# Performance work log

Hardware: AMD Instinct MI355X
Metric: run time of the kernel (lower is better)

## Reference

```python
import jax, jax.numpy as jnp
import numpy as np

B, S, D, H, L, F = 2, 2048, 512, 8, 6, 2048
MAX = 5000
HD = D // H
OFF = MAX - 1


def _layernorm(x, g, b, eps=1e-5):
    m = jnp.mean(x, axis=-1, keepdims=True)
    v = jnp.mean((x - m) ** 2, axis=-1, keepdims=True)
    return (x - m) / jnp.sqrt(v + eps) * g + b


def _sinusoidal_pe(seq_len, d_model):
    pos = jnp.arange(seq_len, dtype=jnp.float32)[:, None]
    div = jnp.exp(jnp.arange(0, d_model, 2, dtype=jnp.float32) * (-np.log(10000.0) / d_model))
    pe = jnp.zeros((seq_len, d_model), jnp.float32)
    pe = pe.at[:, 0::2].set(jnp.sin(pos * div))
    pe = pe.at[:, 1::2].set(jnp.cos(pos * div))
    return pe


def setup_inputs() -> dict:
    key = jax.random.key(0)
    ks = iter(jax.random.split(key, 64))

    def n(shape, s):
        return (jax.random.normal(next(ks), shape, jnp.float32) * s).astype(jnp.float32)

    inp = {}
    inp['x'] = jax.random.normal(next(ks), (B, S, D), jnp.float32)
    inp['f0'] = jax.random.normal(next(ks), (B, S, 1), jnp.float32)
    inp['sp'] = jax.random.normal(next(ks), (B, S, 1), jnp.float32)
    inp['ap'] = jax.random.normal(next(ks), (B, S, 1), jnp.float32)
    inp['spk_emb'] = jax.random.normal(next(ks), (B, D), jnp.float32)
    # conditional positional encoding projections (weights stored as (in,out); y = x @ W + b)
    inp['Wf0'] = n((1, D), 0.1); inp['bf0'] = jnp.zeros((D,), jnp.float32)
    inp['Wsp'] = n((1, D), 0.1); inp['bsp'] = jnp.zeros((D,), jnp.float32)
    inp['Wap'] = n((1, D), 0.1); inp['bap'] = jnp.zeros((D,), jnp.float32)
    inp['Wspk'] = n((D, D), 0.02); inp['bspk'] = jnp.zeros((D,), jnp.float32)
    # per-layer stacked params
    inp['Wq'] = n((L, D, D), 0.02); inp['bq'] = jnp.zeros((L, D), jnp.float32)
    inp['Wk'] = n((L, D, D), 0.02); inp['bk'] = jnp.zeros((L, D), jnp.float32)
    inp['Wv'] = n((L, D, D), 0.02); inp['bv'] = jnp.zeros((L, D), jnp.float32)
    inp['Wo'] = n((L, D, D), 0.02); inp['bo'] = jnp.zeros((L, D), jnp.float32)
    inp['ln1_g'] = jnp.ones((L, D), jnp.float32); inp['ln1_b'] = jnp.zeros((L, D), jnp.float32)
    inp['ln2_g'] = jnp.ones((L, D), jnp.float32); inp['ln2_b'] = jnp.zeros((L, D), jnp.float32)
    inp['W1'] = n((L, D, F), 0.02); inp['b1'] = jnp.zeros((L, F), jnp.float32)
    inp['W2'] = n((L, F, D), 0.02); inp['b2'] = jnp.zeros((L, D), jnp.float32)
    inp['rel_table'] = n((L, 2 * MAX - 1, H), 0.02)
    inp['gfin'] = jnp.ones((D,), jnp.float32); inp['bfin'] = jnp.zeros((D,), jnp.float32)
    return inp


def _forward(x, f0, sp, ap, spk_emb,
             Wf0, bf0, Wsp, bsp, Wap, bap, Wspk, bspk,
             Wq, bq, Wk, bk, Wv, bv, Wo, bo,
             ln1_g, ln1_b, ln2_g, ln2_b, W1, b1, W2, b2,
             rel_table, gfin, bfin):
    # --- conditional positional encoding (dropout = identity, eval mode) ---
    x = x + _sinusoidal_pe(S, D)[None]
    x = x + (f0 @ Wf0 + bf0)
    x = x + (sp @ Wsp + bsp)
    x = x + (ap @ Wap + bap)
    spk = jnp.broadcast_to(spk_emb[:, None, :], (B, S, D))
    x = x + (spk @ Wspk + bspk)

    # relative coords: added bias for (query q, key k) is table[k - q + OFF] (matches transpose(1,3) in torch)
    coords = jnp.arange(S)
    rel = jnp.clip(coords[None, :] - coords[:, None] + OFF, 0, 2 * MAX - 2)  # (S_q, S_k)

    scale = 1.0 / np.sqrt(HD)

    def layer(x, p):
        (Wq_, bq_, Wk_, bk_, Wv_, bv_, Wo_, bo_,
         g1, be1, g2, be2, W1_, b1_, W2_, b2_, tab) = p
        res = x
        h = _layernorm(x, g1, be1)
        Q = (h @ Wq_ + bq_).reshape(B, S, H, HD)
        K = (h @ Wk_ + bk_).reshape(B, S, H, HD)
        V = (h @ Wv_ + bv_).reshape(B, S, H, HD)
        scores = jnp.einsum('bqhd,bkhd->bhqk', Q, K) * scale
        bias = jnp.transpose(tab[rel], (2, 0, 1))  # (H, S_q, S_k)
        scores = scores + bias[None]
        attn = jax.nn.softmax(scores, axis=-1)
        ao = jnp.einsum('bhqk,bkhd->bqhd', attn, V).reshape(B, S, D)
        x = res + (ao @ Wo_ + bo_)
        res = x
        h = _layernorm(x, g2, be2)
        h = jax.nn.gelu(h @ W1_ + b1_, approximate=False)
        x = res + (h @ W2_ + b2_)
        return x, None

    params = (Wq, bq, Wk, bk, Wv, bv, Wo, bo,
              ln1_g, ln1_b, ln2_g, ln2_b, W1, b1, W2, b2, rel_table)
    x, _ = jax.lax.scan(layer, x, params)
    return _layernorm(x, gfin, bfin)


def reference(x, f0, sp, ap, spk_emb,
              Wf0, bf0, Wsp, bsp, Wap, bap, Wspk, bspk,
              Wq, bq, Wk, bk, Wv, bv, Wo, bo,
              ln1_g, ln1_b, ln2_g, ln2_b, W1, b1, W2, b2,
              rel_table, gfin, bfin):
    return _forward(x, f0, sp, ap, spk_emb,
                    Wf0, bf0, Wsp, bsp, Wap, bap, Wspk, bspk,
                    Wq, bq, Wk, bk, Wv, bv, Wo, bo,
                    ln1_g, ln1_b, ln2_g, ln2_b, W1, b1, W2, b2,
                    rel_table, gfin, bfin)
```

## Files before the change

### kernel.cpp

```cpp
#include <hip/hip_runtime.h>
#include <hip/hip_bf16.h>

#define B_ 2
#define S_ 2048
#define D_ 512
#define H_ 8
#define L_ 6
#define F_ 2048
#define HD_ 64
#define M_ 4096
#define OFF_ 4999
#define NREL_ 9999

typedef short s8v __attribute__((ext_vector_type(8)));
typedef float f4v __attribute__((ext_vector_type(4)));

enum { MODE_BF16 = 0, MODE_RES = 1, MODE_GELU = 2 };

__device__ __forceinline__ short f2bf(float f) {
  unsigned u = __float_as_uint(f);
  unsigned r = (u + 0x7fffu + ((u >> 16) & 1u)) >> 16;
  return (short)r;
}

__device__ __forceinline__ float exp2fast(float x) {
  float r;
  asm("v_exp_f32 %0, %1" : "=v"(r) : "v"(x));
  return r;
}

__device__ __forceinline__ int cvt_pk_bf16(float lo, float hi) {
  int r;
  asm("v_cvt_pk_bf16_f32 %0, %1, %2" : "=v"(r) : "v"(lo), "v"(hi));
  return r;
}

__device__ __forceinline__ void gload16(const void* g, const void* l) {
  __builtin_amdgcn_global_load_lds((const __attribute__((address_space(1))) unsigned int*)g,
                                   (__attribute__((address_space(3))) unsigned int*)l,
                                   16, 0, 0);
}

__global__ void transpose_kernel(const float* __restrict__ src, short* __restrict__ dst,
                                 int K, int N, long srcBS, long dstBS, int rowOff)
{
  __shared__ float t[32][33];
  int tx = threadIdx.x, ty = threadIdx.y;
  int n0 = blockIdx.x * 32, k0 = blockIdx.y * 32, l = blockIdx.z;
  const float* s = src + (size_t)l * srcBS;
  short* d = dst + (size_t)l * dstBS;
  for (int j = 0; j < 4; ++j)
    t[ty + j*8][tx] = s[(size_t)(k0 + ty + j*8) * N + n0 + tx];
  __syncthreads();
  for (int j = 0; j < 4; ++j)
    d[(size_t)(rowOff + n0 + ty + j*8) * K + k0 + tx] = f2bf(t[tx][ty + j*8]);
}

__global__ void packb_kernel(const float* __restrict__ bq, const float* __restrict__ bk,
                             const float* __restrict__ bv, float* __restrict__ bqkv)
{
  int i = blockIdx.x * 256 + threadIdx.x;
  if (i >= L_ * 1536) return;
  int l = i / 1536, j = i % 1536;
  float v = (j < 512) ? bq[l*512 + j] : (j < 1024) ? bk[l*512 + j - 512] : bv[l*512 + j - 1024];
  bqkv[i] = v;
}

__global__ void tabt_kernel(const float* __restrict__ tab, float* __restrict__ tabT)
{
  int i = blockIdx.x * 256 + threadIdx.x;
  if (i >= L_ * H_ * NREL_) return;
  int l = i / (H_ * NREL_), rem = i % (H_ * NREL_);
  int h = rem / NREL_, idx = rem % NREL_;
  tabT[i] = tab[((size_t)l * NREL_ + idx) * H_ + h] * 1.44269504f;
}

__global__ __launch_bounds__(256) void spk_kernel(const float* __restrict__ spk,
                                                  const float* __restrict__ Wspk,
                                                  const float* __restrict__ bspk,
                                                  float* __restrict__ sproj)
{
  __shared__ float red[4][64];
  int b = blockIdx.x, nb = blockIdx.y;
  int dl = threadIdx.x & 63, kc = threadIdx.x >> 6;
  int d = nb * 64 + dl;
  const float* sprow = spk + b * D_;
  float a0 = 0.f, a1 = 0.f;
  int kbeg = kc * 128;
  for (int k = kbeg; k < kbeg + 128; k += 2) {
    a0 += sprow[k]     * Wspk[(size_t)k * D_ + d];
    a1 += sprow[k + 1] * Wspk[(size_t)(k + 1) * D_ + d];
  }
  red[kc][dl] = a0 + a1;
  __syncthreads();
  if (kc == 0)
    sproj[b*D_ + d] = red[0][dl] + red[1][dl] + red[2][dl] + red[3][dl] + bspk[d];
}

__global__ __launch_bounds__(256) void prologue_kernel(
    const float* __restrict__ x, const float* __restrict__ f0, const float* __restrict__ sp,
    const float* __restrict__ ap, const float* __restrict__ Wf0, const float* __restrict__ bf0,
    const float* __restrict__ Wsp, const float* __restrict__ bsp,
    const float* __restrict__ Wap, const float* __restrict__ bap,
    const float* __restrict__ sproj, float* __restrict__ X)
{
  int row = blockIdx.x, tid = threadIdx.x;
  int b = row >> 11, s = row & 2047;
  float vf0 = f0[row], vsp = sp[row], vap = ap[row];
  for (int j = 0; j < 2; ++j) {
    int d = tid + j * 256;
    int i = d >> 1;
    float div = expf((float)(2*i) * -0.01798894603f);
    float arg = (float)s * div;
    float pe = (d & 1) ? cosf(arg) : sinf(arg);
    float v = x[(size_t)row*D_ + d] + pe
            + vf0*Wf0[d] + bf0[d] + vsp*Wsp[d] + bsp[d] + vap*Wap[d] + bap[d]
            + sproj[b*D_ + d];
    X[(size_t)row*D_ + d] = v;
  }
}

__global__ __launch_bounds__(256) void ln_kernel(
    const float* __restrict__ X, const float* __restrict__ g, const float* __restrict__ bta,
    short* __restrict__ outB, float* __restrict__ outF, int f32out)
{
  __shared__ float red[8];
  int row = blockIdx.x, tid = threadIdx.x;
  const float* xr = X + (size_t)row * D_;
  float v0 = xr[tid], v1 = xr[tid + 256];
  float s = v0 + v1, q = v0*v0 + v1*v1;
  for (int off = 1; off < 64; off <<= 1) { s += __shfl_xor(s, off); q += __shfl_xor(q, off); }
  int w = tid >> 6;
  if ((tid & 63) == 0) { red[w*2] = s; red[w*2 + 1] = q; }
  __syncthreads();
  s = red[0] + red[2] + red[4] + red[6];
  q = red[1] + red[3] + red[5] + red[7];
  float mean = s * (1.0f / D_);
  float var = q * (1.0f / D_) - mean * mean;
  float rstd = rsqrtf(var + 1e-5f);
  float o0 = (v0 - mean) * rstd * g[tid] + bta[tid];
  float o1 = (v1 - mean) * rstd * g[tid + 256] + bta[tid + 256];
  if (f32out) {
    outF[(size_t)row*D_ + tid] = o0; outF[(size_t)row*D_ + tid + 256] = o1;
  } else {
    outB[(size_t)row*D_ + tid] = f2bf(o0); outB[(size_t)row*D_ + tid + 256] = f2bf(o1);
  }
}

template<int MODE>
__device__ __forceinline__ void gemm_body(
    const short* __restrict__ A, const short* __restrict__ Wt,
    const float* __restrict__ bias, int K, int N,
    float* outF, short* outB)
{
  __shared__ short sA[2][4096];
  __shared__ short sB[2][2048];
  const int tid = threadIdx.x;
  const int w = tid >> 6, lane = tid & 63;
  const int col = lane & 15, quad = lane >> 4;
  const int m0 = blockIdx.x * 128, n0 = blockIdx.y * 64;
  const int nkt = K >> 6;

  const int rowT = tid >> 2, kcA = tid & 3;
  const size_t kc8 = kcA * 8;

  f4v acc[2][4] = {};
  for (int kt = 0; kt < nkt; ++kt) {
    const int k0 = kt * 64;
    __syncthreads();
    for (int p = 0; p < 2; ++p) {
      gload16(A + (size_t)(m0 + rowT) * K + k0 + p*32 + kc8,       &sA[p][(w*16) * 32]);
      gload16(A + (size_t)(m0 + 64 + rowT) * K + k0 + p*32 + kc8,  &sA[p][(64 + w*16) * 32]);
      gload16(Wt + (size_t)(n0 + rowT) * K + k0 + p*32 + kc8,      &sB[p][(w*16) * 32]);
    }
    __syncthreads();
    for (int p = 0; p < 2; ++p) {
      s8v af[2], bfr[4];
      for (int mt = 0; mt < 2; ++mt)
        af[mt] = *(const s8v*)&sA[p][(w*32 + mt*16 + col) * 32 + quad * 8];
      for (int nt = 0; nt < 4; ++nt)
        bfr[nt] = *(const s8v*)&sB[p][(nt*16 + col) * 32 + quad * 8];
      for (int mt = 0; mt < 2; ++mt)
        for (int nt = 0; nt < 4; ++nt)
          acc[mt][nt] = __builtin_amdgcn_mfma_f32_16x16x32_bf16(af[mt], bfr[nt], acc[mt][nt], 0, 0, 0);
    }
  }

  const float qsc = (MODE == MODE_BF16 && n0 < 512) ? 0.18033688f : 1.0f;
  float bz[4];
  for (int nt = 0; nt < 4; ++nt)
    bz[nt] = bias[n0 + nt*16 + col];
  for (int mt = 0; mt < 2; ++mt) {
    int mbase = m0 + w*32 + mt*16 + quad*4;
    for (int nt = 0; nt < 4; ++nt) {
      int n = n0 + nt*16 + col;
      for (int r = 0; r < 4; ++r) {
        float v = acc[mt][nt][r] + bz[nt];
        size_t idx = (size_t)(mbase + r) * N + n;
        if (MODE == MODE_RES) {
          outF[idx] = outF[idx] + v;
        } else if (MODE == MODE_GELU) {
          outB[idx] = f2bf(0.5f * v * (1.0f + erff(v * 0.70710678118f)));
        } else {
          outB[idx] = f2bf(v * qsc);
        }
      }
    }
  }
}

__global__ __launch_bounds__(256) void gemm_qkv_kernel(
    const short* __restrict__ A, const short* __restrict__ Wt,
    const float* __restrict__ bias, float* outF, short* outB)
{ gemm_body<MODE_BF16>(A, Wt, bias, 512, 1536, outF, outB); }

__global__ __launch_bounds__(256) void gemm_o_kernel(
    const short* __restrict__ A, const short* __restrict__ Wt,
    const float* __restrict__ bias, float* outF, short* outB)
{ gemm_body<MODE_RES>(A, Wt, bias, 512, 512, outF, outB); }

__global__ __launch_bounds__(256) void gemm_ffn1_kernel(
    const short* __restrict__ A, const short* __restrict__ Wt,
    const float* __restrict__ bias, float* outF, short* outB)
{ gemm_body<MODE_GELU>(A, Wt, bias, 512, 2048, outF, outB); }

__global__ __launch_bounds__(256) void gemm_ffn2_kernel(
    const short* __restrict__ A, const short* __restrict__ Wt,
    const float* __restrict__ bias, float* outF, short* outB)
{ gemm_body<MODE_RES>(A, Wt, bias, 2048, 512, outF, outB); }

__global__ __launch_bounds__(256) void vtrans_kernel(const short* __restrict__ QKV,
                                                     short* __restrict__ Vt)
{
  __shared__ short t[64 * 72];
  int tid = threadIdx.x;
  int s0 = blockIdx.x * 64, bh = blockIdx.y;
  int b = bh >> 3, h = bh & 7;
  for (int it = 0; it < 2; ++it) {
    int c = it * 256 + tid;
    int sR = c >> 3, hc = c & 7;
    s8v v = *(const s8v*)(QKV + (size_t)(b*S_ + s0 + sR) * 1536 + 1024 + h*64 + hc*8);
    *(s8v*)&t[sR * 72 + hc * 8] = v;
  }
  __syncthreads();
  for (int it = 0; it < 2; ++it) {
    int c = it * 256 + tid;
    int hd = c >> 3, sc = c & 7;
    s8v v;
    for (int j = 0; j < 8; ++j) v[j] = t[(sc*8 + j) * 72 + hd];
    *(s8v*)(Vt + (size_t)(bh*64 + hd) * S_ + s0 + sc*8) = v;
  }
}

#define SM_MT(ko, mt, ST, Bb0, Bb1, Bb2, Bb3) do {                  \
    float p0 = exp2fast(ST[0] + Bb0);                               \
    float p1 = exp2fast(ST[1] + Bb1);                               \
    float p2 = exp2fast(ST[2] + Bb2);                               \
    float p3 = exp2fast(ST[3] + Bb3);                               \
    lsum += (p0 + p1) + (p2 + p3);                                  \
    int2 pk;                                                        \
    pk.x = cvt_pk_bf16(p0, p1);                                     \
    pk.y = cvt_pk_bf16(p2, p3);                                     \
    *(int2*)&sP[w*1280 + (ko)*640 + col*40 + (mt)*16 + quad*4] = pk;\
  } while (0)

#define KOBLOCK(ko, B0a,B0b,B0c,B0d, B1a,B1b,B1c,B1d) do {                         \
    f4v st0 = {}, st1 = {};                                                        \
    s8v a00 = *(const s8v*)&sK[(ko)*2560 + 0*1280 + (0*16 + col)*40 + quad*8];     \
    s8v a01 = *(const s8v*)&sK[(ko)*2560 + 1*1280 + (0*16 + col)*40 + quad*8];     \
    s8v a10 = *(const s8v*)&sK[(ko)*2560 + 0*1280 + (1*16 + col)*40 + quad*8];     \
    s8v a11 = *(const s8v*)&sK[(ko)*2560 + 1*1280 + (1*16 + col)*40 + quad*8];     \
    st0 = __builtin_amdgcn_mfma_f32_16x16x32_bf16(a00, bQ0, st0, 0, 0, 0);         \
    st0 = __builtin_amdgcn_mfma_f32_16x16x32_bf16(a01, bQ1, st0, 0, 0, 0);         \
    st1 = __builtin_amdgcn_mfma_f32_16x16x32_bf16(a10, bQ0, st1, 0, 0, 0);         \
    st1 = __builtin_amdgcn_mfma_f32_16x16x32_bf16(a11, bQ1, st1, 0, 0, 0);         \
    SM_MT(ko, 0, st0, B0a,B0b,B0c,B0d);                                            \
    SM_MT(ko, 1, st1, B1a,B1b,B1c,B1d);                                            \
    s8v aP = *(const s8v*)&sP[w*1280 + (ko)*640 + col*40 + quad*8];                \
    s8v v0 = *(const s8v*)&sV[(ko)*2560 + ( 0 + col)*40 + quad*8];                 \
    s8v v1 = *(const s8v*)&sV[(ko)*2560 + (16 + col)*40 + quad*8];                 \
    s8v v2 = *(const s8v*)&sV[(ko)*2560 + (32 + col)*40 + quad*8];                 \
    s8v v3 = *(const s8v*)&sV[(ko)*2560 + (48 + col)*40 + quad*8];                 \
    o0 = __builtin_amdgcn_mfma_f32_16x16x32_bf16(aP, v0, o0, 0, 0, 0);             \
    o1 = __builtin_amdgcn_mfma_f32_16x16x32_bf16(aP, v1, o1, 0, 0, 0);             \
    o2 = __builtin_amdgcn_mfma_f32_16x16x32_bf16(aP, v2, o2, 0, 0, 0);             \
    o3 = __builtin_amdgcn_mfma_f32_16x16x32_bf16(aP, v3, o3, 0, 0, 0);             \
  } while (0)

__global__ __launch_bounds__(512) void flash_kernel(
    const short* __restrict__ QKV, const short* __restrict__ Vt,
    const float* __restrict__ tabT, short* __restrict__ AO)
{
  __shared__ __attribute__((aligned(16))) short sK[2 * 2 * 32 * 40];
  __shared__ __attribute__((aligned(16))) short sV[2 * 64 * 40];
  __shared__ __attribute__((aligned(16))) short sP[8 * 2 * 16 * 40];
  __shared__ float sRow[8 * 16];

  const int tid = threadIdx.x;
  const int w = tid >> 6, lane = tid & 63;
  const int col = lane & 15, quad = lane >> 4;
  const int bh = blockIdx.x, qt = blockIdx.y;
  const int b = bh >> 3, h = bh & 7;
  const int q0 = qt * 128;
  const int wq = w * 16;
  const int nkt = S_ / 64;
  const float* tabh = tabT + (size_t)h * NREL_;
  const float* tbL = tabh + (OFF_ - q0 + quad*4 - wq - col);

  const short* gQ = QKV + (size_t)(b*S_ + q0 + wq + col) * 1536 + h*64 + quad*8;
  s8v bQ0 = *(const s8v*)gQ;
  s8v bQ1 = *(const s8v*)(gQ + 32);

  const int c4 = tid & 3;
  const int kK = (tid >> 2) & 63, hcK = tid >> 8;
  const short* gK = QKV + (size_t)(b*S_ + kK) * 1536 + 512 + h*64 + hcK*32 + c4*8;
  short* dK = &sK[(kK >> 5)*2560 + hcK*1280 + (kK & 31)*40 + c4*8];
  const int c8 = tid & 7, hdV = tid >> 3;
  const short* gV = Vt + (size_t)(bh*64 + hdV) * S_ + c8*8;
  short* dV = &sV[(c8 >> 2)*2560 + hdV*40 + (c8 & 3)*8];

  int4 rk = *(const int4*)gK;
  int4 rv = *(const int4*)gV;

  float lsum = 0.0f;
  f4v o0 = {}, o1 = {}, o2 = {}, o3 = {};

  for (int kt = 0; kt < nkt; ++kt) {
    const float* tb = tbL + kt * 64;
    float bA0 = tb[0],  bA1 = tb[1],  bA2 = tb[2],  bA3 = tb[3];
    float bB0 = tb[16], bB1 = tb[17], bB2 = tb[18], bB3 = tb[19];
    float bC0 = tb[32], bC1 = tb[33], bC2 = tb[34], bC3 = tb[35];
    float bD0 = tb[48], bD1 = tb[49], bD2 = tb[50], bD3 = tb[51];
    __syncthreads();
    *(int4*)dK = rk;
    *(int4*)dV = rv;
    __syncthreads();
    if (kt + 1 < nkt) {
      rk = *(const int4*)(gK + (size_t)(kt + 1) * 64 * 1536);
      rv = *(const int4*)(gV + (kt + 1) * 64);
    }
    KOBLOCK(0, bA0, bA1, bA2, bA3, bB0, bB1, bB2, bB3);
    KOBLOCK(1, bC0, bC1, bC2, bC3, bD0, bD1, bD2, bD3);
  }

  lsum += __shfl_xor(lsum, 16);
  lsum += __shfl_xor(lsum, 32);
  if (lane < 16) sRow[w*16 + lane] = lsum;
  float rs0 = sRow[w*16 + quad*4 + 0];
  float rs1 = sRow[w*16 + quad*4 + 1];
  float rs2 = sRow[w*16 + quad*4 + 2];
  float rs3 = sRow[w*16 + quad*4 + 3];
  size_t mrow = (size_t)(b*S_ + q0 + wq + quad*4);
  short* aoBase = AO + mrow * 512 + h*64 + col;
  aoBase[0*512 +  0] = f2bf(o0[0] / rs0);
  aoBase[1*512 +  0] = f2bf(o0[1] / rs1);
  aoBase[2*512 +  0] = f2bf(o0[2] / rs2);
  aoBase[3*512 +  0] = f2bf(o0[3] / rs3);
  aoBase[0*512 + 16] = f2bf(o1[0] / rs0);
  aoBase[1*512 + 16] = f2bf(o1[1] / rs1);
  aoBase[2*512 + 16] = f2bf(o1[2] / rs2);
  aoBase[3*512 + 16] = f2bf(o1[3] / rs3);
  aoBase[0*512 + 32] = f2bf(o2[0] / rs0);
  aoBase[1*512 + 32] = f2bf(o2[1] / rs1);
  aoBase[2*512 + 32] = f2bf(o2[2] / rs2);
  aoBase[3*512 + 32] = f2bf(o2[3] / rs3);
  aoBase[0*512 + 48] = f2bf(o3[0] / rs0);
  aoBase[1*512 + 48] = f2bf(o3[1] / rs1);
  aoBase[2*512 + 48] = f2bf(o3[2] / rs2);
  aoBase[3*512 + 48] = f2bf(o3[3] / rs3);
}

extern "C" void kernel_launch(void* const* d_in, const int* in_sizes, int n_in,
                              void* d_out, int out_size, void* d_ws, size_t ws_size,
                              hipStream_t stream)
{
  const float* x    = (const float*)d_in[0];
  const float* f0   = (const float*)d_in[1];
  const float* sp   = (const float*)d_in[2];
  const float* ap   = (const float*)d_in[3];
  const float* spk  = (const float*)d_in[4];
  const float* Wf0  = (const float*)d_in[5];  const float* bf0  = (const float*)d_in[6];
  const float* Wsp  = (const float*)d_in[7];  const float* bsp  = (const float*)d_in[8];
  const float* Wap  = (const float*)d_in[9];  const float* bap  = (const float*)d_in[10];
  const float* Wspk = (const float*)d_in[11]; const float* bspk = (const float*)d_in[12];
  const float* Wq   = (const float*)d_in[13]; const float* bq   = (const float*)d_in[14];
  const float* Wk   = (const float*)d_in[15]; const float* bk   = (const float*)d_in[16];
  const float* Wv   = (const float*)d_in[17]; const float* bv   = (const float*)d_in[18];
  const float* Wo   = (const float*)d_in[19]; const float* bo   = (const float*)d_in[20];
  const float* ln1g = (const float*)d_in[21]; const float* ln1b = (const float*)d_in[22];
  const float* ln2g = (const float*)d_in[23]; const float* ln2b = (const float*)d_in[24];
  const float* W1   = (const float*)d_in[25]; const float* b1   = (const float*)d_in[26];
  const float* W2   = (const float*)d_in[27]; const float* b2   = (const float*)d_in[28];
  const float* tab  = (const float*)d_in[29];
  const float* gfin = (const float*)d_in[30]; const float* bfin = (const float*)d_in[31];

  char* p = (char*)d_ws;
  auto alloc = [&](size_t bytes) { char* r = p; p += (bytes + 255) & ~(size_t)255; return r; };
  short* WqkvT = (short*)alloc((size_t)L_ * 1536 * 512 * 2);
  short* WoT   = (short*)alloc((size_t)L_ * 512 * 512 * 2);
  short* W1T   = (short*)alloc((size_t)L_ * 2048 * 512 * 2);
  short* W2T   = (short*)alloc((size_t)L_ * 512 * 2048 * 2);
  float* bqkv  = (float*)alloc((size_t)L_ * 1536 * 4);
  float* X     = (float*)alloc((size_t)M_ * D_ * 4);
  short* Hb    = (short*)alloc((size_t)M_ * D_ * 2);
  short* AO    = (short*)alloc((size_t)M_ * D_ * 2);
  short* QKVb  = (short*)alloc((size_t)M_ * 1536 * 2);
  short* VtG   = (short*)alloc((size_t)B_ * H_ * HD_ * S_ * 2);
  short* H1b   = QKVb;
  float* sproj = (float*)alloc((size_t)B_ * D_ * 4);
  float* tabT  = (float*)alloc((size_t)L_ * H_ * NREL_ * 4);

  dim3 b256(256);
  dim3 tb(32, 8);
  packb_kernel<<<dim3((L_*1536 + 255)/256), b256, 0, stream>>>(bq, bk, bv, bqkv);
  tabt_kernel<<<dim3((L_*H_*NREL_ + 255)/256), b256, 0, stream>>>(tab, tabT);
  transpose_kernel<<<dim3(16, 16, L_), tb, 0, stream>>>(Wq, WqkvT, 512, 512, 512*512, 1536*512, 0);
  transpose_kernel<<<dim3(16, 16, L_), tb, 0, stream>>>(Wk, WqkvT, 512, 512, 512*512, 1536*512, 512);
  transpose_kernel<<<dim3(16, 16, L_), tb, 0, stream>>>(Wv, WqkvT, 512, 512, 512*512, 1536*512, 1024);
  transpose_kernel<<<dim3(16, 16, L_), tb, 0, stream>>>(Wo, WoT, 512, 512, 512*512, 512*512, 0);
  transpose_kernel<<<dim3(64, 16, L_), tb, 0, stream>>>(W1, W1T, 512, 2048, 512*2048, 2048*512, 0);
  transpose_kernel<<<dim3(16, 64, L_), tb, 0, stream>>>(W2, W2T, 2048, 512, 2048*512, 512*2048, 0);
  spk_kernel<<<dim3(B_, 8), b256, 0, stream>>>(spk, Wspk, bspk, sproj);
  prologue_kernel<<<dim3(M_), b256, 0, stream>>>(x, f0, sp, ap, Wf0, bf0, Wsp, bsp, Wap, bap, sproj, X);

  for (int l = 0; l < L_; ++l) {
    ln_kernel<<<dim3(M_), b256, 0, stream>>>(X, ln1g + l*D_, ln1b + l*D_, Hb, nullptr, 0);
    gemm_qkv_kernel<<<dim3(32, 24, 1), b256, 0, stream>>>(
        Hb, WqkvT + (size_t)l*1536*512, bqkv + l*1536, nullptr, QKVb);
    vtrans_kernel<<<dim3(S_/64, B_*H_), b256, 0, stream>>>(QKVb, VtG);
    flash_kernel<<<dim3(B_*H_, S_/128), dim3(512), 0, stream>>>(QKVb, VtG, tabT + (size_t)l*H_*NREL_, AO);
    gemm_o_kernel<<<dim3(32, 8, 1), b256, 0, stream>>>(
        AO, WoT + (size_t)l*512*512, bo + l*D_, X, nullptr);
    ln_kernel<<<dim3(M_), b256, 0, stream>>>(X, ln2g + l*D_, ln2b + l*D_, Hb, nullptr, 0);
    gemm_ffn1_kernel<<<dim3(32, 32, 1), b256, 0, stream>>>(
        Hb, W1T + (size_t)l*2048*512, b1 + l*F_, nullptr, H1b);
    gemm_ffn2_kernel<<<dim3(32, 8, 1), b256, 0, stream>>>(
        H1b, W2T + (size_t)l*512*2048, b2 + l*D_, X, nullptr);
  }
  ln_kernel<<<dim3(M_), b256, 0, stream>>>(X, gfin, bfin, nullptr, (float*)d_out, 1);
}
```

Baseline: 917.4 us.

## Split flash attention warps into two key-teams each covering 32 query rows

Reorganizes the flash attention block so its 8 waves form two teams. Each team handles one 32-key half of every 64-key tile, and each wave covers 32 query rows instead of 16. Every K and V fragment loaded from shared memory now feeds two query subtiles, which halves LDS reads per MFMA and reuses the bias loads. The two teams' partial outputs and row sums are combined through shared memory at the end, which costs an extra barrier, more accumulator registers and a reduction step.

```diff
diff --git a/kernel.cpp b/kernel.cpp
--- a/kernel.cpp
+++ b/kernel.cpp
@@ -252,85 +252,69 @@
   }
 }
 
-#define SM_MT(ko, mt, ST, Bb0, Bb1, Bb2, Bb3) do {                  \
-    float p0 = exp2fast(ST[0] + Bb0);                               \
-    float p1 = exp2fast(ST[1] + Bb1);                               \
-    float p2 = exp2fast(ST[2] + Bb2);                               \
-    float p3 = exp2fast(ST[3] + Bb3);                               \
-    lsum += (p0 + p1) + (p2 + p3);                                  \
+#define SM2(ST, Ba, Bb, Bc, Bd, LS, slotQ, kpos) do {               \
+    float p0 = exp2fast(ST[0] + Ba);                                \
+    float p1 = exp2fast(ST[1] + Bb);                                \
+    float p2 = exp2fast(ST[2] + Bc);                                \
+    float p3 = exp2fast(ST[3] + Bd);                                \
+    LS += (p0 + p1) + (p2 + p3);                                    \
     int2 pk;                                                        \
     pk.x = cvt_pk_bf16(p0, p1);                                     \
     pk.y = cvt_pk_bf16(p2, p3);                                     \
-    *(int2*)&sP[w*1280 + (ko)*640 + col*40 + (mt)*16 + quad*4] = pk;\
+    *(int2*)&sAll[10240 + w*1280 + (slotQ)*640 + col*40 + (kpos) + quad*4] = pk; \
   } while (0)
 
-#define KOBLOCK(ko, B0a,B0b,B0c,B0d, B1a,B1b,B1c,B1d) do {                         \
-    f4v st0 = {}, st1 = {};                                                        \
-    s8v a00 = *(const s8v*)&sK[(ko)*2560 + 0*1280 + (0*16 + col)*40 + quad*8];     \
-    s8v a01 = *(const s8v*)&sK[(ko)*2560 + 1*1280 + (0*16 + col)*40 + quad*8];     \
-    s8v a10 = *(const s8v*)&sK[(ko)*2560 + 0*1280 + (1*16 + col)*40 + quad*8];     \
-    s8v a11 = *(const s8v*)&sK[(ko)*2560 + 1*1280 + (1*16 + col)*40 + quad*8];     \
-    st0 = __builtin_amdgcn_mfma_f32_16x16x32_bf16(a00, bQ0, st0, 0, 0, 0);         \
-    st0 = __builtin_amdgcn_mfma_f32_16x16x32_bf16(a01, bQ1, st0, 0, 0, 0);         \
-    st1 = __builtin_amdgcn_mfma_f32_16x16x32_bf16(a10, bQ0, st1, 0, 0, 0);         \
-    st1 = __builtin_amdgcn_mfma_f32_16x16x32_bf16(a11, bQ1, st1, 0, 0, 0);         \
-    SM_MT(ko, 0, st0, B0a,B0b,B0c,B0d);                                            \
-    SM_MT(ko, 1, st1, B1a,B1b,B1c,B1d);                                            \
-    s8v aP = *(const s8v*)&sP[w*1280 + (ko)*640 + col*40 + quad*8];                \
-    s8v v0 = *(const s8v*)&sV[(ko)*2560 + ( 0 + col)*40 + quad*8];                 \
-    s8v v1 = *(const s8v*)&sV[(ko)*2560 + (16 + col)*40 + quad*8];                 \
-    s8v v2 = *(const s8v*)&sV[(ko)*2560 + (32 + col)*40 + quad*8];                 \
-    s8v v3 = *(const s8v*)&sV[(ko)*2560 + (48 + col)*40 + quad*8];                 \
-    o0 = __builtin_amdgcn_mfma_f32_16x16x32_bf16(aP, v0, o0, 0, 0, 0);             \
-    o1 = __builtin_amdgcn_mfma_f32_16x16x32_bf16(aP, v1, o1, 0, 0, 0);             \
-    o2 = __builtin_amdgcn_mfma_f32_16x16x32_bf16(aP, v2, o2, 0, 0, 0);             \
-    o3 = __builtin_amdgcn_mfma_f32_16x16x32_bf16(aP, v3, o3, 0, 0, 0);             \
-  } while (0)
+#define MFMA16(A, Bv, C) C = __builtin_amdgcn_mfma_f32_16x16x32_bf16(A, Bv, C, 0, 0, 0)
 
 __global__ __launch_bounds__(512) void flash_kernel(
     const short* __restrict__ QKV, const short* __restrict__ Vt,
     const float* __restrict__ tabT, short* __restrict__ AO)
 {
-  __shared__ __attribute__((aligned(16))) short sK[2 * 2 * 32 * 40];
-  __shared__ __attribute__((aligned(16))) short sV[2 * 64 * 40];
-  __shared__ __attribute__((aligned(16))) short sP[8 * 2 * 16 * 40];
-  __shared__ float sRow[8 * 16];
+  __shared__ __attribute__((aligned(16))) short sAll[20480];
+  __shared__ float sRowA[256];
 
   const int tid = threadIdx.x;
   const int w = tid >> 6, lane = tid & 63;
   const int col = lane & 15, quad = lane >> 4;
+  const int team = w >> 2, qg = w & 3;
+  const int qbase = qg * 32;
   const int bh = blockIdx.x, qt = blockIdx.y;
   const int b = bh >> 3, h = bh & 7;
   const int q0 = qt * 128;
-  const int wq = w * 16;
   const int nkt = S_ / 64;
   const float* tabh = tabT + (size_t)h * NREL_;
-  const float* tbL = tabh + (OFF_ - q0 + quad*4 - wq - col);
-
-  const short* gQ = QKV + (size_t)(b*S_ + q0 + wq + col) * 1536 + h*64 + quad*8;
-  s8v bQ0 = *(const s8v*)gQ;
-  s8v bQ1 = *(const s8v*)(gQ + 32);
+  const float* tbB = tabh + (OFF_ - q0 - qbase - col + team*32 + quad*4);
+
+  const short* gQ0 = QKV + (size_t)(b*S_ + q0 + qbase + col) * 1536 + h*64 + quad*8;
+  s8v bQ00 = *(const s8v*)gQ0;
+  s8v bQ01 = *(const s8v*)(gQ0 + 32);
+  const short* gQ1 = gQ0 + 16*1536;
+  s8v bQ10 = *(const s8v*)gQ1;
+  s8v bQ11 = *(const s8v*)(gQ1 + 32);
 
   const int c4 = tid & 3;
   const int kK = (tid >> 2) & 63, hcK = tid >> 8;
   const short* gK = QKV + (size_t)(b*S_ + kK) * 1536 + 512 + h*64 + hcK*32 + c4*8;
-  short* dK = &sK[(kK >> 5)*2560 + hcK*1280 + (kK & 31)*40 + c4*8];
+  short* dK = &sAll[(kK >> 5)*2560 + hcK*1280 + (kK & 31)*40 + c4*8];
   const int c8 = tid & 7, hdV = tid >> 3;
   const short* gV = Vt + (size_t)(bh*64 + hdV) * S_ + c8*8;
-  short* dV = &sV[(c8 >> 2)*2560 + hdV*40 + (c8 & 3)*8];
+  short* dV = &sAll[5120 + (c8 >> 2)*2560 + hdV*40 + (c8 & 3)*8];
 
   int4 rk = *(const int4*)gK;
   int4 rv = *(const int4*)gV;
 
-  float lsum = 0.0f;
-  f4v o0 = {}, o1 = {}, o2 = {}, o3 = {};
+  float lsum0 = 0.0f, lsum1 = 0.0f;
+  f4v o00 = {}, o01 = {}, o02 = {}, o03 = {};
+  f4v o10 = {}, o11 = {}, o12 = {}, o13 = {};
+
+  const int kofs = team * 2560;
+  const int vofs = 5120 + team * 2560;
 
   for (int kt = 0; kt < nkt; ++kt) {
-    const float* tb = tbL + kt * 64;
-    float bA0 = tb[0],  bA1 = tb[1],  bA2 = tb[2],  bA3 = tb[3];
-    float bB0 = tb[16], bB1 = tb[17], bB2 = tb[18], bB3 = tb[19];
-    float bC0 = tb[32], bC1 = tb[33], bC2 = tb[34], bC3 = tb[35];
-    float bD0 = tb[48], bD1 = tb[49], bD2 = tb[50], bD3 = tb[51];
+    const float* tb = tbB + kt * 64;
+    float bm0 = tb[-16], bm1 = tb[-15], bm2 = tb[-14], bm3 = tb[-13];
+    float b00 = tb[0],   b01 = tb[1],   b02 = tb[2],   b03 = tb[3];
+    float bp0 = tb[16],  bp1 = tb[17],  bp2 = tb[18],  bp3 = tb[19];
     __syncthreads();
     *(int4*)dK = rk;
     *(int4*)dV = rv;
@@ -339,35 +323,78 @@
       rk = *(const int4*)(gK + (size_t)(kt + 1) * 64 * 1536);
       rv = *(const int4*)(gV + (kt + 1) * 64);
     }
-    KOBLOCK(0, bA0, bA1, bA2, bA3, bB0, bB1, bB2, bB3);
-    KOBLOCK(1, bC0, bC1, bC2, bC3, bD0, bD1, bD2, bD3);
-  }
-
-  lsum += __shfl_xor(lsum, 16);
-  lsum += __shfl_xor(lsum, 32);
-  if (lane < 16) sRow[w*16 + lane] = lsum;
-  float rs0 = sRow[w*16 + quad*4 + 0];
-  float rs1 = sRow[w*16 + quad*4 + 1];
-  float rs2 = sRow[w*16 + quad*4 + 2];
-  float rs3 = sRow[w*16 + quad*4 + 3];
-  size_t mrow = (size_t)(b*S_ + q0 + wq + quad*4);
-  short* aoBase = AO + mrow * 512 + h*64 + col;
-  aoBase[0*512 +  0] = f2bf(o0[0] / rs0);
-  aoBase[1*512 +  0] = f2bf(o0[1] / rs1);
-  aoBase[2*512 +  0] = f2bf(o0[2] / rs2);
-  aoBase[3*512 +  0] = f2bf(o0[3] / rs3);
-  aoBase[0*512 + 16] = f2bf(o1[0] / rs0);
-  aoBase[1*512 + 16] = f2bf(o1[1] / rs1);
-  aoBase[2*512 + 16] = f2bf(o1[2] / rs2);
-  aoBase[3*512 + 16] = f2bf(o1[3] / rs3);
-  aoBase[0*512 + 32] = f2bf(o2[0] / rs0);
-  aoBase[1*512 + 32] = f2bf(o2[1] / rs1);
-  aoBase[2*512 + 32] = f2bf(o2[2] / rs2);
-  aoBase[3*512 + 32] = f2bf(o2[3] / rs3);
-  aoBase[0*512 + 48] = f2bf(o3[0] / rs0);
-  aoBase[1*512 + 48] = f2bf(o3[1] / rs1);
-  aoBase[2*512 + 48] = f2bf(o3[2] / rs2);
-  aoBase[3*512 + 48] = f2bf(o3[3] / rs3);
+    s8v ak00 = *(const s8v*)&sAll[kofs + 0*1280 + ( 0 + col)*40 + quad*8];
+    s8v ak01 = *(const s8v*)&sAll[kofs + 1*1280 + ( 0 + col)*40 + quad*8];
+    s8v ak10 = *(const s8v*)&sAll[kofs + 0*1280 + (16 + col)*40 + quad*8];
+    s8v ak11 = *(const s8v*)&sAll[kofs + 1*1280 + (16 + col)*40 + quad*8];
+    f4v st00 = {}, st01 = {}, st10 = {}, st11 = {};
+    MFMA16(ak00, bQ00, st00); MFMA16(ak01, bQ01, st00);
+    MFMA16(ak00, bQ10, st01); MFMA16(ak01, bQ11, st01);
+    MFMA16(ak10, bQ00, st10); MFMA16(ak11, bQ01, st10);
+    MFMA16(ak10, bQ10, st11); MFMA16(ak11, bQ11, st11);
+    SM2(st00, b00, b01, b02, b03, lsum0, 0, 0);
+    SM2(st01, bm0, bm1, bm2, bm3, lsum1, 1, 0);
+    SM2(st10, bp0, bp1, bp2, bp3, lsum0, 0, 16);
+    SM2(st11, b00, b01, b02, b03, lsum1, 1, 16);
+    s8v aP0 = *(const s8v*)&sAll[10240 + w*1280 +   0 + col*40 + quad*8];
+    s8v aP1 = *(const s8v*)&sAll[10240 + w*1280 + 640 + col*40 + quad*8];
+    s8v bv0 = *(const s8v*)&sAll[vofs + ( 0 + col)*40 + quad*8];
+    s8v bv1 = *(const s8v*)&sAll[vofs + (16 + col)*40 + quad*8];
+    s8v bv2 = *(const s8v*)&sAll[vofs + (32 + col)*40 + quad*8];
+    s8v bv3 = *(const s8v*)&sAll[vofs + (48 + col)*40 + quad*8];
+    MFMA16(aP0, bv0, o00); MFMA16(aP0, bv1, o01);
+    MFMA16(aP0, bv2, o02); MFMA16(aP0, bv3, o03);
+    MFMA16(aP1, bv0, o10); MFMA16(aP1, bv1, o11);
+    MFMA16(aP1, bv2, o12); MFMA16(aP1, bv3, o13);
+  }
+
+  lsum0 += __shfl_xor(lsum0, 16); lsum0 += __shfl_xor(lsum0, 32);
+  lsum1 += __shfl_xor(lsum1, 16); lsum1 += __shfl_xor(lsum1, 32);
+  __syncthreads();
+  if (lane < 16) {
+    sRowA[team*128 + qg*32 + lane]      = lsum0;
+    sRowA[team*128 + qg*32 + 16 + lane] = lsum1;
+  }
+  f4v* sComb = (f4v*)sAll;
+  if (team == 1) {
+    sComb[(qg*8 + 0)*64 + lane] = o00;
+    sComb[(qg*8 + 1)*64 + lane] = o01;
+    sComb[(qg*8 + 2)*64 + lane] = o02;
+    sComb[(qg*8 + 3)*64 + lane] = o03;
+    sComb[(qg*8 + 4)*64 + lane] = o10;
+    sComb[(qg*8 + 5)*64 + lane] = o11;
+    sComb[(qg*8 + 6)*64 + lane] = o12;
+    sComb[(qg*8 + 7)*64 + lane] = o13;
+  }
+  __syncthreads();
+  if (team == 0) {
+    int rbase = qg*32 + quad*4;
+    float ra0 = sRowA[rbase+0] + sRowA[128+rbase+0];
+    float ra1 = sRowA[rbase+1] + sRowA[128+rbase+1];
+    float ra2 = sRowA[rbase+2] + sRowA[128+rbase+2];
+    float ra3 = sRowA[rbase+3] + sRowA[128+rbase+3];
+    float rb0 = sRowA[rbase+16+0] + sRowA[128+rbase+16+0];
+    float rb1 = sRowA[rbase+16+1] + sRowA[128+rbase+16+1];
+    float rb2 = sRowA[rbase+16+2] + sRowA[128+rbase+16+2];
+    float rb3 = sRowA[rbase+16+3] + sRowA[128+rbase+16+3];
+    short* aoRow = AO + (size_t)(b*S_ + q0 + qbase)*512 + h*64 + col;
+#define WOUT(OV, qg2, nt, RA0, RA1, RA2, RA3) do {                       \
+      f4v pp = OV + sComb[(qg*8 + (qg2)*4 + (nt))*64 + lane];            \
+      aoRow[((qg2)*16 + quad*4 + 0)*512 + (nt)*16] = f2bf(pp[0] / RA0);  \
+      aoRow[((qg2)*16 + quad*4 + 1)*512 + (nt)*16] = f2bf(pp[1] / RA1);  \
+      aoRow[((qg2)*16 + quad*4 + 2)*512 + (nt)*16] = f2bf(pp[2] / RA2);  \
+      aoRow[((qg2)*16 + quad*4 + 3)*512 + (nt)*16] = f2bf(pp[3] / RA3);  \
+    } while (0)
+    WOUT(o00, 0, 0, ra0, ra1, ra2, ra3);
+    WOUT(o01, 0, 1, ra0, ra1, ra2, ra3);
+    WOUT(o02, 0, 2, ra0, ra1, ra2, ra3);
+    WOUT(o03, 0, 3, ra0, ra1, ra2, ra3);
+    WOUT(o10, 1, 0, rb0, rb1, rb2, rb3);
+    WOUT(o11, 1, 1, rb0, rb1, rb2, rb3);
+    WOUT(o12, 1, 2, rb0, rb1, rb2, rb3);
+    WOUT(o13, 1, 3, rb0, rb1, rb2, rb3);
+#undef WOUT
+  }
 }
 
 extern "C" void kernel_launch(void* const* d_in, const int* in_sizes, int n_in,
```

Result: no change. 911.8 us (-0.6%).
